# Optimization experiments

Measured on AMD Instinct MI355X. Metric: run time of the kernel, lower is better.

## Reference

```python
import jax, jax.numpy as jnp
import numpy as np

EPS = 1e-5  # config.layer_norm_epsilon

def setup_inputs() -> dict:
    key = jax.random.key(0)
    ks = jax.random.split(key, 8)
    B, S, D, BOT, N = 8, 2048, 1024, 400, 25
    x = jax.random.normal(ks[0], (B, S, D), dtype=jnp.float32)
    alphas = jax.random.uniform(ks[1], (N,), dtype=jnp.float32) / N
    W_down_all = jax.random.normal(ks[2], (N, BOT, D), dtype=jnp.float32) * 0.02
    W_up_all = jax.random.normal(ks[3], (N, D, BOT), dtype=jnp.float32) * 0.02
    b_down_all = jax.random.normal(ks[4], (N, BOT), dtype=jnp.float32) * 0.02
    b_up_all = jax.random.normal(ks[5], (N, D), dtype=jnp.float32) * 0.02
    W_ln_all = 1.0 + jax.random.normal(ks[6], (N, D), dtype=jnp.float32) * 0.02
    b_ln_all = jax.random.normal(ks[7], (N, D), dtype=jnp.float32) * 0.02
    return {"x": x, "alphas": alphas, "W_down_all": W_down_all, "W_up_all": W_up_all,
            "b_down_all": b_down_all, "b_up_all": b_up_all,
            "W_ln_all": W_ln_all, "b_ln_all": b_ln_all}

def reference(x, alphas, W_down_all, W_up_all, b_down_all, b_up_all, W_ln_all, b_ln_all):
    # Superposition: alpha-weighted sum of all adapters' parameters
    # (original python loop over 25 adapters -> single einsum per tensor).
    W_down = jnp.einsum('n,nbd->bd', alphas, W_down_all)  # [BOT, D]
    W_up   = jnp.einsum('n,ndb->db', alphas, W_up_all)    # [D, BOT]
    W_ln   = jnp.einsum('n,nd->d',  alphas, W_ln_all)     # [D]
    b_ln   = jnp.einsum('n,nd->d',  alphas, b_ln_all)     # [D]
    # b_up / b_down are merged in the original too but passed with bias=None: unused.

    # FAdapter: F.layer_norm with normalized_shape = x.shape[1:], i.e. normalize
    # jointly over (seq, embd) per batch element; ln weight/bias broadcast over seq.
    mu = jnp.mean(x, axis=(1, 2), keepdims=True)
    var = jnp.mean(jnp.square(x - mu), axis=(1, 2), keepdims=True)
    x_ = (x - mu) * jax.lax.rsqrt(var + EPS) * W_ln + b_ln  # [B,S,D]

    h = jax.nn.relu(jnp.einsum('bsd,od->bso', x_, W_down))  # [B,S,BOT], no bias
    x_ = jnp.einsum('bso,do->bsd', h, W_up)                 # [B,S,D],   no bias
    return x + x_
```

## Files before the change

### kernel.cpp

```cpp
#include <hip/hip_runtime.h>
#include <stdint.h>

#define NB   8
#define SS   2048
#define DD   1024
#define BOT  400
#define BOTP 512
#define NAD  25
#define LN_EPS 1e-5f
#define NCH  128

typedef __attribute__((ext_vector_type(8))) short bf8_t;
typedef __attribute__((ext_vector_type(4))) float fx4;

__device__ __forceinline__ unsigned short f2bf(float f) {
  unsigned int u = __float_as_uint(f);
  u = (u + 0x7FFFu + ((u >> 16) & 1u)) >> 16;
  return (unsigned short)u;
}
__device__ __forceinline__ uint32_t cvtpk(float lo, float hi) {
  uint32_t r;
  asm("v_cvt_pk_bf16_f32 %0, %1, %2" : "=v"(r) : "v"(lo), "v"(hi));
  return r;
}

__device__ __forceinline__ void gload16(void* lds, const void* g) {
  __builtin_amdgcn_global_load_lds(
      (const __attribute__((address_space(1))) void*)(uintptr_t)g,
      (__attribute__((address_space(3))) void*)(uint32_t)(uintptr_t)lds,
      16, 0, 0);
}

__global__ __launch_bounds__(256) void mix_kernel(
    const float* __restrict__ alphas,
    const float* __restrict__ WdAll, const float* __restrict__ WuAll,
    const float* __restrict__ wlnAll, const float* __restrict__ blnAll,
    unsigned short* __restrict__ Wd, unsigned short* __restrict__ Wu,
    float* __restrict__ wln, float* __restrict__ bln)
{
  __shared__ float a[NAD];
  const int tid = threadIdx.x;
  if (tid < NAD) a[tid] = alphas[tid];
  __syncthreads();
  const int bid = blockIdx.x;

  if (bid < 800) {
    const int g = (bid < 400 ? bid : bid - 400) * 256 + tid;
    const float4* src = (const float4*)(bid < 400 ? WdAll : WuAll) + g;
    float4 vals[NAD];
#pragma unroll
    for (int n = 0; n < NAD; ++n) vals[n] = src[(size_t)n * 102400];
    float4 acc = {0.f, 0.f, 0.f, 0.f};
#pragma unroll
    for (int n = 0; n < NAD; ++n) {
      acc.x += a[n] * vals[n].x; acc.y += a[n] * vals[n].y;
      acc.z += a[n] * vals[n].z; acc.w += a[n] * vals[n].w;
    }
    uint2 pk = { cvtpk(acc.x, acc.y), cvtpk(acc.z, acc.w) };
    if (bid < 400) {
      *(uint2*)(Wd + (size_t)g * 4) = pk;
    } else {
      const int d = g / 100, bg = g - d * 100;
      *(uint2*)(Wu + (size_t)d * BOTP + bg * 4) = pk;
    }
  } else if (bid < 808) {
    const int i = (bid - 800) * 256 + tid;
    const float* src = (i < DD) ? wlnAll : blnAll;
    const int j = (i < DD) ? i : (i - DD);
    float v[NAD];
#pragma unroll
    for (int n = 0; n < NAD; ++n) v[n] = src[(size_t)n * DD + j];
    float s = 0.f;
#pragma unroll
    for (int n = 0; n < NAD; ++n) s += a[n] * v[n];
    if (i < DD) wln[j] = s; else bln[j] = s;
  } else if (bid < 864) {
    const int t = (bid - 808) * 256 + tid;
    int4 z = {0, 0, 0, 0};
    *(int4*)(Wd + 400 * 1024 + (size_t)t * 8) = z;
  } else {
    const int t = (bid - 864) * 256 + tid;
    const int row = t / 14, c8 = t - row * 14;
    int4 z = {0, 0, 0, 0};
    *(int4*)(Wu + (size_t)row * BOTP + 400 + c8 * 8) = z;
  }
}

__global__ __launch_bounds__(256) void stats_kernel(const float* __restrict__ x,
                                                    float* __restrict__ partials)
{
  const int b = blockIdx.y, c = blockIdx.x;
  const float4* xb = (const float4*)(x + (size_t)b * SS * DD) + (size_t)c * 4096;
  float s = 0.f, q = 0.f;
#pragma unroll 4
  for (int i = threadIdx.x; i < 4096; i += 256) {
    float4 v = xb[i];
    s += v.x + v.y + v.z + v.w;
    q += v.x * v.x + v.y * v.y + v.z * v.z + v.w * v.w;
  }
#pragma unroll
  for (int off = 32; off > 0; off >>= 1) { s += __shfl_down(s, off); q += __shfl_down(q, off); }
  __shared__ float red[8];
  const int wave = threadIdx.x >> 6, lane = threadIdx.x & 63;
  if (!lane) { red[wave] = s; red[wave + 4] = q; }
  __syncthreads();
  if (!threadIdx.x) {
    partials[(b * NCH + c) * 2]     = red[0] + red[1] + red[2] + red[3];
    partials[(b * NCH + c) * 2 + 1] = red[4] + red[5] + red[6] + red[7];
  }
}

__global__ __launch_bounds__(256) void gemm1(
    const float* __restrict__ x, const unsigned short* __restrict__ Bw,
    const float* __restrict__ partials, const float* __restrict__ wln,
    const float* __restrict__ bln, unsigned short* __restrict__ H)
{
  __shared__ unsigned short As[2][128 * 64];
  __shared__ unsigned short Bs[2][128 * 64];
  __shared__ float s1[DD], s2[DD];
  const int tid = threadIdx.x, wave = tid >> 6, lane = tid & 63;
  const int wr = wave >> 1, wc = wave & 1;
  const int bid = (blockIdx.x & 7) * 64 + (blockIdx.x >> 3);
  const int bcol = bid & 3, brow = bid >> 2;
  const int b = brow >> 4;

  double sd = 0.0, qd = 0.0;
#pragma unroll 8
  for (int i = 0; i < NCH; ++i) {
    sd += partials[(b * NCH + i) * 2];
    qd += partials[(b * NCH + i) * 2 + 1];
  }
  const float mu  = (float)(sd * (1.0 / 2097152.0));
  const float var = (float)(qd * (1.0 / 2097152.0)) - mu * mu;
  const float rs  = rsqrtf(var + LN_EPS);
  for (int c = tid; c < DD; c += 256) {
    const float v1 = rs * wln[c];
    s1[c] = v1; s2[c] = bln[c] - mu * v1;
  }

  const float* Ab = x + (size_t)(brow * 128) * DD;
  const unsigned short* Bb = Bw + (size_t)(bcol * 128) * DD;
  const int arow = tid >> 3;
  const int c8   = tid & 7;
  const int aswz = (arow & 7) << 4;

  auto loadA = [&](int k0, float4* xr) {
#pragma unroll
    for (int i = 0; i < 4; ++i) {
      const float* p = Ab + (size_t)(i * 32 + arow) * DD + k0 + c8 * 8;
      xr[i * 2]     = *(const float4*)p;
      xr[i * 2 + 1] = *(const float4*)(p + 4);
    }
  };
  auto writeA = [&](int buf, int k0, const float4* xr) {
    const float4 w0 = *(const float4*)&s1[k0 + c8 * 8];
    const float4 w1 = *(const float4*)&s1[k0 + c8 * 8 + 4];
    const float4 b0 = *(const float4*)&s2[k0 + c8 * 8];
    const float4 b1 = *(const float4*)&s2[k0 + c8 * 8 + 4];
#pragma unroll
    for (int i = 0; i < 4; ++i) {
      const float4 v0 = xr[i * 2], v1 = xr[i * 2 + 1];
      uint4 pk;
      pk.x = cvtpk(v0.x * w0.x + b0.x, v0.y * w0.y + b0.y);
      pk.y = cvtpk(v0.z * w0.z + b0.z, v0.w * w0.w + b0.w);
      pk.z = cvtpk(v1.x * w1.x + b1.x, v1.y * w1.y + b1.y);
      pk.w = cvtpk(v1.z * w1.z + b1.z, v1.w * w1.w + b1.w);
      *(uint4*)((char*)&As[buf][0] + (i * 32 + arow) * 128 + ((c8 * 16) ^ aswz)) = pk;
    }
  };
  auto stageB = [&](int buf, int k0) {
#pragma unroll
    for (int i = 0; i < 4; ++i) {
      const int q   = i * 256 + wave * 64;
      const int ql  = q + lane;
      const int row = ql >> 3, c16 = ql & 7;
      const int o   = c16 ^ (row & 7);
      gload16(&Bs[buf][q * 8], Bb + (size_t)row * DD + k0 + o * 8);
    }
  };

  fx4 acc[4][4] = {};
  auto compute = [&](int buf) {
#pragma unroll
    for (int kk = 0; kk < 2; ++kk) {
      bf8_t af[4], bf[4];
#pragma unroll
      for (int m = 0; m < 4; ++m) {
        const int r = wr * 64 + m * 16 + (lane & 15);
        af[m] = *(const bf8_t*)((const char*)&As[buf][0] + r * 128 +
                                ((kk * 64 + (lane >> 4) * 16) ^ ((r & 7) << 4)));
      }
#pragma unroll
      for (int n = 0; n < 4; ++n) {
        const int r = wc * 64 + n * 16 + (lane & 15);
        bf[n] = *(const bf8_t*)((const char*)&Bs[buf][0] + r * 128 +
                                ((kk * 64 + (lane >> 4) * 16) ^ ((r & 7) << 4)));
      }
#pragma unroll
      for (int m = 0; m < 4; ++m)
#pragma unroll
        for (int n = 0; n < 4; ++n)
          acc[m][n] = __builtin_amdgcn_mfma_f32_16x16x32_bf16(af[m], bf[n], acc[m][n], 0, 0, 0);
    }
  };

  float4 xrA[8], xrB[8];
  loadA(0, xrA); stageB(0, 0);
  __syncthreads();
  writeA(0, 0, xrA);
  __syncthreads();
#pragma unroll 1
  for (int t2 = 0; t2 < 8; ++t2) {
    {
      const int t = t2 * 2;
      if (t < 15) { loadA((t + 1) * 64, xrB); stageB(1, (t + 1) * 64); }
      compute(0);
      if (t < 15) writeA(1, (t + 1) * 64, xrB);
      __syncthreads();
    }
    {
      const int t = t2 * 2 + 1;
      if (t < 15) { loadA((t + 1) * 64, xrA); stageB(0, (t + 1) * 64); }
      compute(1);
      if (t < 15) writeA(0, (t + 1) * 64, xrA);
      __syncthreads();
    }
  }

  unsigned short* Hs = &As[0][0];
  const int r0l = wr * 64 + ((lane >> 4) << 2);
  const int c0l = wc * 64 + (lane & 15);
#pragma unroll
  for (int m = 0; m < 4; ++m)
#pragma unroll
    for (int n = 0; n < 4; ++n)
#pragma unroll
      for (int j = 0; j < 4; ++j) {
        float v = acc[m][n][j];
        Hs[(r0l + m * 16 + j) * 128 + (c0l + n * 16)] = f2bf(v > 0.f ? v : 0.f);
      }
  __syncthreads();
  const size_t outbase = (size_t)(brow * 128) * BOTP + (size_t)bcol * 128;
#pragma unroll
  for (int i = 0; i < 8; ++i) {
    const int idx = i * 256 + tid;
    const int row = idx >> 4, colg = idx & 15;
    *(int4*)(H + outbase + (size_t)row * BOTP + colg * 8) = *(const int4*)&Hs[row * 128 + colg * 8];
  }
}

__global__ __launch_bounds__(256) void gemm2(
    const unsigned short* __restrict__ A, const unsigned short* __restrict__ Bm,
    const float* __restrict__ Xres, float* __restrict__ out)
{
  __shared__ unsigned short As[2][128 * 32];
  __shared__ unsigned short Bs[2][128 * 32];
  const int tid = threadIdx.x, wave = tid >> 6, lane = tid & 63;
  const int wr = wave >> 1, wc = wave & 1;
  const int bid = (blockIdx.x & 7) * 128 + (blockIdx.x >> 3);
  const int bcol = bid & 7, brow = bid >> 3;
  const unsigned short* Ab = A + (size_t)(brow * 128) * BOTP;
  const unsigned short* Bb = Bm + (size_t)(bcol * 128) * BOTP;

  auto stage = [&](int buf, int k0) {
#pragma unroll
    for (int i = 0; i < 2; ++i) {
      const int q   = i * 256 + wave * 64;
      const int ql  = q + lane;
      const int row = ql >> 2, c16 = ql & 3;
      const int o   = c16 ^ (row & 3);
      gload16(&As[buf][q * 8], Ab + (size_t)row * BOTP + k0 + o * 8);
      gload16(&Bs[buf][q * 8], Bb + (size_t)row * BOTP + k0 + o * 8);
    }
  };

  fx4 acc[4][4] = {};
  stage(0, 0);
  __syncthreads();
  for (int t = 0; t < 16; ++t) {
    const int cur = t & 1;
    if (t < 15) stage(cur ^ 1, (t + 1) * 32);
    bf8_t af[4], bf[4];
    const int hi16 = (lane >> 4) * 16;
#pragma unroll
    for (int m = 0; m < 4; ++m) {
      const int r = wr * 64 + m * 16 + (lane & 15);
      af[m] = *(const bf8_t*)((const char*)&As[cur][0] + r * 64 + (hi16 ^ ((r & 3) << 4)));
    }
#pragma unroll
    for (int n = 0; n < 4; ++n) {
      const int r = wc * 64 + n * 16 + (lane & 15);
      bf[n] = *(const bf8_t*)((const char*)&Bs[cur][0] + r * 64 + (hi16 ^ ((r & 3) << 4)));
    }
#pragma unroll
    for (int m = 0; m < 4; ++m)
#pragma unroll
      for (int n = 0; n < 4; ++n)
        acc[m][n] = __builtin_amdgcn_mfma_f32_16x16x32_bf16(af[m], bf[n], acc[m][n], 0, 0, 0);
    __syncthreads();
  }

  const int r0 = brow * 128 + wr * 64 + ((lane >> 4) << 2);
  const int c0 = bcol * 128 + wc * 64 + (lane & 15);
#pragma unroll
  for (int m = 0; m < 4; ++m)
#pragma unroll
    for (int n = 0; n < 4; ++n)
#pragma unroll
      for (int j = 0; j < 4; ++j) {
        const size_t off = (size_t)(r0 + m * 16 + j) * DD + (c0 + n * 16);
        out[off] = acc[m][n][j] + Xres[off];
      }
}

extern "C" void kernel_launch(void* const* d_in, const int* in_sizes, int n_in,
                              void* d_out, int out_size, void* d_ws, size_t ws_size,
                              hipStream_t stream)
{
  const float* x      = (const float*)d_in[0];
  const float* alphas = (const float*)d_in[1];
  const float* WdAll  = (const float*)d_in[2];
  const float* WuAll  = (const float*)d_in[3];
  const float* wlnAll = (const float*)d_in[6];
  const float* blnAll = (const float*)d_in[7];
  float* out = (float*)d_out;

  char* ws = (char*)d_ws;
  unsigned short* Wd  = (unsigned short*)ws;
  unsigned short* Wu  = (unsigned short*)(ws + (1u << 20));
  float* wln          = (float*)(ws + (2u << 20));
  float* bln          = wln + DD;
  float* partials     = bln + DD;
  unsigned short* h   = (unsigned short*)(ws + (3u << 20));

  mix_kernel<<<920, 256, 0, stream>>>(alphas, WdAll, WuAll, wlnAll, blnAll, Wd, Wu, wln, bln);
  stats_kernel<<<dim3(NCH, NB), 256, 0, stream>>>(x, partials);
  gemm1<<<512, 256, 0, stream>>>(x, Wd, partials, wln, bln, h);
  gemm2<<<1024, 256, 0, stream>>>(h, Wu, x, out);
}
```

Before: 274.7 us.

## Fuse mix and stats kernels, shrink GEMM K-tiles, drop swizzle and remapping

Merges the weight-mixing and LayerNorm statistics kernels into one launch so the x reduction and the adapter mixing share a grid. gemm1 moves from a 64-wide double-buffered K tile to a 32-wide single-buffered LDS tile with register prefetch of A. gemm2 becomes single-buffered with a sync per K step. Both GEMMs lose their XOR LDS swizzle and their XCD-aware block remapping. These changes cut launches and LDS footprint but risk bank conflicts, more barriers and worse L2 locality.

```diff
diff --git a/kernel.cpp b/kernel.cpp
--- a/kernel.cpp
+++ b/kernel.cpp
@@ -31,18 +31,45 @@
       16, 0, 0);
 }
 
-__global__ __launch_bounds__(256) void mix_kernel(
+__global__ __launch_bounds__(256) void mixstats_kernel(
     const float* __restrict__ alphas,
     const float* __restrict__ WdAll, const float* __restrict__ WuAll,
     const float* __restrict__ wlnAll, const float* __restrict__ blnAll,
+    const float* __restrict__ x,
     unsigned short* __restrict__ Wd, unsigned short* __restrict__ Wu,
-    float* __restrict__ wln, float* __restrict__ bln)
+    float* __restrict__ wln, float* __restrict__ bln,
+    float* __restrict__ partials)
 {
+  const int tid = threadIdx.x;
+  const int bid = blockIdx.x;
+
+  if (bid >= 920) {
+    const int g = bid - 920;
+    const int b = g >> 7, c = g & 127;
+    const float4* xb = (const float4*)(x + (size_t)b * SS * DD) + (size_t)c * 4096;
+    float s = 0.f, q = 0.f;
+#pragma unroll 4
+    for (int i = tid; i < 4096; i += 256) {
+      float4 v = xb[i];
+      s += v.x + v.y + v.z + v.w;
+      q += v.x * v.x + v.y * v.y + v.z * v.z + v.w * v.w;
+    }
+#pragma unroll
+    for (int off = 32; off > 0; off >>= 1) { s += __shfl_down(s, off); q += __shfl_down(q, off); }
+    __shared__ float red[8];
+    const int wave = tid >> 6, lane = tid & 63;
+    if (!lane) { red[wave] = s; red[wave + 4] = q; }
+    __syncthreads();
+    if (!tid) {
+      partials[(b * NCH + c) * 2]     = red[0] + red[1] + red[2] + red[3];
+      partials[(b * NCH + c) * 2 + 1] = red[4] + red[5] + red[6] + red[7];
+    }
+    return;
+  }
+
   __shared__ float a[NAD];
-  const int tid = threadIdx.x;
   if (tid < NAD) a[tid] = alphas[tid];
   __syncthreads();
-  const int bid = blockIdx.x;
 
   if (bid < 800) {
     const int g = (bid < 400 ? bid : bid - 400) * 256 + tid;
@@ -86,42 +113,20 @@
   }
 }
 
-__global__ __launch_bounds__(256) void stats_kernel(const float* __restrict__ x,
-                                                    float* __restrict__ partials)
-{
-  const int b = blockIdx.y, c = blockIdx.x;
-  const float4* xb = (const float4*)(x + (size_t)b * SS * DD) + (size_t)c * 4096;
-  float s = 0.f, q = 0.f;
-#pragma unroll 4
-  for (int i = threadIdx.x; i < 4096; i += 256) {
-    float4 v = xb[i];
-    s += v.x + v.y + v.z + v.w;
-    q += v.x * v.x + v.y * v.y + v.z * v.z + v.w * v.w;
-  }
-#pragma unroll
-  for (int off = 32; off > 0; off >>= 1) { s += __shfl_down(s, off); q += __shfl_down(q, off); }
-  __shared__ float red[8];
-  const int wave = threadIdx.x >> 6, lane = threadIdx.x & 63;
-  if (!lane) { red[wave] = s; red[wave + 4] = q; }
-  __syncthreads();
-  if (!threadIdx.x) {
-    partials[(b * NCH + c) * 2]     = red[0] + red[1] + red[2] + red[3];
-    partials[(b * NCH + c) * 2 + 1] = red[4] + red[5] + red[6] + red[7];
-  }
-}
-
 __global__ __launch_bounds__(256) void gemm1(
-    const float* __restrict__ x, const unsigned short* __restrict__ Bw,
+    const float* __restrict__ x, const unsigned short* __restrict__ Wdm,
     const float* __restrict__ partials, const float* __restrict__ wln,
     const float* __restrict__ bln, unsigned short* __restrict__ H)
 {
-  __shared__ unsigned short As[2][128 * 64];
-  __shared__ unsigned short Bs[2][128 * 64];
-  __shared__ float s1[DD], s2[DD];
+  __shared__ char smraw[32768];
+  unsigned short* As = (unsigned short*)smraw;
+  unsigned short* Bs = (unsigned short*)(smraw + 8192);
+  float* s1 = (float*)(smraw + 16384);
+  float* s2 = (float*)(smraw + 20480);
+
   const int tid = threadIdx.x, wave = tid >> 6, lane = tid & 63;
   const int wr = wave >> 1, wc = wave & 1;
-  const int bid = (blockIdx.x & 7) * 64 + (blockIdx.x >> 3);
-  const int bcol = bid & 3, brow = bid >> 2;
+  const int bcol = blockIdx.x & 3, brow = blockIdx.x >> 2;
   const int b = brow >> 4;
 
   double sd = 0.0, qd = 0.0;
@@ -139,95 +144,91 @@
   }
 
   const float* Ab = x + (size_t)(brow * 128) * DD;
-  const unsigned short* Bb = Bw + (size_t)(bcol * 128) * DD;
-  const int arow = tid >> 3;
-  const int c8   = tid & 7;
-  const int aswz = (arow & 7) << 4;
+  const unsigned short* Bb = Wdm + (size_t)(bcol * 128) * DD;
+  const int row2 = tid >> 1;
+  const int c16  = (tid & 1) * 16;
 
   auto loadA = [&](int k0, float4* xr) {
-#pragma unroll
-    for (int i = 0; i < 4; ++i) {
-      const float* p = Ab + (size_t)(i * 32 + arow) * DD + k0 + c8 * 8;
-      xr[i * 2]     = *(const float4*)p;
-      xr[i * 2 + 1] = *(const float4*)(p + 4);
-    }
+    const float* p = Ab + (size_t)row2 * DD + k0 + c16;
+    xr[0] = *(const float4*)p;     xr[1] = *(const float4*)(p + 4);
+    xr[2] = *(const float4*)(p + 8); xr[3] = *(const float4*)(p + 12);
   };
-  auto writeA = [&](int buf, int k0, const float4* xr) {
-    const float4 w0 = *(const float4*)&s1[k0 + c8 * 8];
-    const float4 w1 = *(const float4*)&s1[k0 + c8 * 8 + 4];
-    const float4 b0 = *(const float4*)&s2[k0 + c8 * 8];
-    const float4 b1 = *(const float4*)&s2[k0 + c8 * 8 + 4];
-#pragma unroll
-    for (int i = 0; i < 4; ++i) {
-      const float4 v0 = xr[i * 2], v1 = xr[i * 2 + 1];
-      uint4 pk;
-      pk.x = cvtpk(v0.x * w0.x + b0.x, v0.y * w0.y + b0.y);
-      pk.y = cvtpk(v0.z * w0.z + b0.z, v0.w * w0.w + b0.w);
-      pk.z = cvtpk(v1.x * w1.x + b1.x, v1.y * w1.y + b1.y);
-      pk.w = cvtpk(v1.z * w1.z + b1.z, v1.w * w1.w + b1.w);
-      *(uint4*)((char*)&As[buf][0] + (i * 32 + arow) * 128 + ((c8 * 16) ^ aswz)) = pk;
-    }
+  auto writeA = [&](int k0, const float4* xr) {
+    const float4 wA = *(const float4*)&s1[k0 + c16],      wB = *(const float4*)&s1[k0 + c16 + 4];
+    const float4 wC = *(const float4*)&s1[k0 + c16 + 8],  wD = *(const float4*)&s1[k0 + c16 + 12];
+    const float4 bA = *(const float4*)&s2[k0 + c16],      bB = *(const float4*)&s2[k0 + c16 + 4];
+    const float4 bC = *(const float4*)&s2[k0 + c16 + 8],  bD = *(const float4*)&s2[k0 + c16 + 12];
+    uint4 p0, p1;
+    p0.x = cvtpk(xr[0].x * wA.x + bA.x, xr[0].y * wA.y + bA.y);
+    p0.y = cvtpk(xr[0].z * wA.z + bA.z, xr[0].w * wA.w + bA.w);
+    p0.z = cvtpk(xr[1].x * wB.x + bB.x, xr[1].y * wB.y + bB.y);
+    p0.w = cvtpk(xr[1].z * wB.z + bB.z, xr[1].w * wB.w + bB.w);
+    p1.x = cvtpk(xr[2].x * wC.x + bC.x, xr[2].y * wC.y + bC.y);
+    p1.y = cvtpk(xr[2].z * wC.z + bC.z, xr[2].w * wC.w + bC.w);
+    p1.z = cvtpk(xr[3].x * wD.x + bD.x, xr[3].y * wD.y + bD.y);
+    p1.w = cvtpk(xr[3].z * wD.z + bD.z, xr[3].w * wD.w + bD.w);
+    *(uint4*)&As[row2 * 32 + c16]     = p0;
+    *(uint4*)&As[row2 * 32 + c16 + 8] = p1;
   };
-  auto stageB = [&](int buf, int k0) {
-#pragma unroll
-    for (int i = 0; i < 4; ++i) {
-      const int q   = i * 256 + wave * 64;
-      const int ql  = q + lane;
-      const int row = ql >> 3, c16 = ql & 7;
-      const int o   = c16 ^ (row & 7);
-      gload16(&Bs[buf][q * 8], Bb + (size_t)row * DD + k0 + o * 8);
+  auto stageB = [&](int k0) {
+#pragma unroll
+    for (int i = 0; i < 2; ++i) {
+      const int basee = (i * 256 + wave * 64) * 8;
+      const int e   = basee + lane * 8;
+      const int row = e >> 5, col = e & 31;
+      gload16(&Bs[basee], Bb + (size_t)row * DD + k0 + col);
     }
   };
 
   fx4 acc[4][4] = {};
-  auto compute = [&](int buf) {
-#pragma unroll
-    for (int kk = 0; kk < 2; ++kk) {
-      bf8_t af[4], bf[4];
-#pragma unroll
-      for (int m = 0; m < 4; ++m) {
-        const int r = wr * 64 + m * 16 + (lane & 15);
-        af[m] = *(const bf8_t*)((const char*)&As[buf][0] + r * 128 +
-                                ((kk * 64 + (lane >> 4) * 16) ^ ((r & 7) << 4)));
-      }
-#pragma unroll
-      for (int n = 0; n < 4; ++n) {
-        const int r = wc * 64 + n * 16 + (lane & 15);
-        bf[n] = *(const bf8_t*)((const char*)&Bs[buf][0] + r * 128 +
-                                ((kk * 64 + (lane >> 4) * 16) ^ ((r & 7) << 4)));
-      }
-#pragma unroll
-      for (int m = 0; m < 4; ++m)
-#pragma unroll
-        for (int n = 0; n < 4; ++n)
-          acc[m][n] = __builtin_amdgcn_mfma_f32_16x16x32_bf16(af[m], bf[n], acc[m][n], 0, 0, 0);
-    }
+  auto compute = [&]() {
+    bf8_t af[4], bf[4];
+    const int hi8 = (lane >> 4) * 8;
+#pragma unroll
+    for (int m = 0; m < 4; ++m)
+      af[m] = *(const bf8_t*)&As[(wr * 64 + m * 16 + (lane & 15)) * 32 + hi8];
+#pragma unroll
+    for (int n = 0; n < 4; ++n)
+      bf[n] = *(const bf8_t*)&Bs[(wc * 64 + n * 16 + (lane & 15)) * 32 + hi8];
+#pragma unroll
+    for (int m = 0; m < 4; ++m)
+#pragma unroll
+      for (int n = 0; n < 4; ++n)
+        acc[m][n] = __builtin_amdgcn_mfma_f32_16x16x32_bf16(af[m], bf[n], acc[m][n], 0, 0, 0);
   };
 
-  float4 xrA[8], xrB[8];
-  loadA(0, xrA); stageB(0, 0);
+  float4 xrA[4], xrB[4];
+  loadA(0, xrA); stageB(0); loadA(32, xrB);
   __syncthreads();
-  writeA(0, 0, xrA);
+  writeA(0, xrA);
   __syncthreads();
 #pragma unroll 1
-  for (int t2 = 0; t2 < 8; ++t2) {
+  for (int t2 = 0; t2 < 16; ++t2) {
     {
       const int t = t2 * 2;
-      if (t < 15) { loadA((t + 1) * 64, xrB); stageB(1, (t + 1) * 64); }
-      compute(0);
-      if (t < 15) writeA(1, (t + 1) * 64, xrB);
+      compute();
+      __syncthreads();
+      if (t < 31) {
+        stageB((t + 1) * 32);
+        writeA((t + 1) * 32, xrB);
+        if (t + 2 < 32) loadA((t + 2) * 32, xrA);
+      }
       __syncthreads();
     }
     {
       const int t = t2 * 2 + 1;
-      if (t < 15) { loadA((t + 1) * 64, xrA); stageB(0, (t + 1) * 64); }
-      compute(1);
-      if (t < 15) writeA(0, (t + 1) * 64, xrA);
+      compute();
       __syncthreads();
-    }
-  }
-
-  unsigned short* Hs = &As[0][0];
+      if (t < 31) {
+        stageB((t + 1) * 32);
+        writeA((t + 1) * 32, xrA);
+        if (t + 2 < 32) loadA((t + 2) * 32, xrB);
+      }
+      __syncthreads();
+    }
+  }
+
+  unsigned short* Hs = (unsigned short*)smraw;
   const int r0l = wr * 64 + ((lane >> 4) << 2);
   const int c0l = wc * 64 + (lane & 15);
 #pragma unroll
@@ -253,45 +254,33 @@
     const unsigned short* __restrict__ A, const unsigned short* __restrict__ Bm,
     const float* __restrict__ Xres, float* __restrict__ out)
 {
-  __shared__ unsigned short As[2][128 * 32];
-  __shared__ unsigned short Bs[2][128 * 32];
+  __shared__ unsigned short As[128 * 32];
+  __shared__ unsigned short Bs[128 * 32];
   const int tid = threadIdx.x, wave = tid >> 6, lane = tid & 63;
   const int wr = wave >> 1, wc = wave & 1;
-  const int bid = (blockIdx.x & 7) * 128 + (blockIdx.x >> 3);
-  const int bcol = bid & 7, brow = bid >> 3;
+  const int bcol = blockIdx.x & 7, brow = blockIdx.x >> 3;
   const unsigned short* Ab = A + (size_t)(brow * 128) * BOTP;
   const unsigned short* Bb = Bm + (size_t)(bcol * 128) * BOTP;
 
-  auto stage = [&](int buf, int k0) {
+  fx4 acc[4][4] = {};
+  for (int k0 = 0; k0 < 512; k0 += 32) {
 #pragma unroll
     for (int i = 0; i < 2; ++i) {
-      const int q   = i * 256 + wave * 64;
-      const int ql  = q + lane;
-      const int row = ql >> 2, c16 = ql & 3;
-      const int o   = c16 ^ (row & 3);
-      gload16(&As[buf][q * 8], Ab + (size_t)row * BOTP + k0 + o * 8);
-      gload16(&Bs[buf][q * 8], Bb + (size_t)row * BOTP + k0 + o * 8);
-    }
-  };
-
-  fx4 acc[4][4] = {};
-  stage(0, 0);
-  __syncthreads();
-  for (int t = 0; t < 16; ++t) {
-    const int cur = t & 1;
-    if (t < 15) stage(cur ^ 1, (t + 1) * 32);
+      const int basee = (i * 256 + wave * 64) * 8;
+      const int e   = basee + lane * 8;
+      const int row = e >> 5, col = e & 31;
+      gload16(&As[basee], Ab + (size_t)row * BOTP + k0 + col);
+      gload16(&Bs[basee], Bb + (size_t)row * BOTP + k0 + col);
+    }
+    __syncthreads();
     bf8_t af[4], bf[4];
-    const int hi16 = (lane >> 4) * 16;
-#pragma unroll
-    for (int m = 0; m < 4; ++m) {
-      const int r = wr * 64 + m * 16 + (lane & 15);
-      af[m] = *(const bf8_t*)((const char*)&As[cur][0] + r * 64 + (hi16 ^ ((r & 3) << 4)));
-    }
-#pragma unroll
-    for (int n = 0; n < 4; ++n) {
-      const int r = wc * 64 + n * 16 + (lane & 15);
-      bf[n] = *(const bf8_t*)((const char*)&Bs[cur][0] + r * 64 + (hi16 ^ ((r & 3) << 4)));
-    }
+    const int hi8 = (lane >> 4) * 8;
+#pragma unroll
+    for (int m = 0; m < 4; ++m)
+      af[m] = *(const bf8_t*)&As[(wr * 64 + m * 16 + (lane & 15)) * 32 + hi8];
+#pragma unroll
+    for (int n = 0; n < 4; ++n)
+      bf[n] = *(const bf8_t*)&Bs[(wc * 64 + n * 16 + (lane & 15)) * 32 + hi8];
 #pragma unroll
     for (int m = 0; m < 4; ++m)
 #pragma unroll
@@ -333,8 +322,8 @@
   float* partials     = bln + DD;
   unsigned short* h   = (unsigned short*)(ws + (3u << 20));
 
-  mix_kernel<<<920, 256, 0, stream>>>(alphas, WdAll, WuAll, wlnAll, blnAll, Wd, Wu, wln, bln);
-  stats_kernel<<<dim3(NCH, NB), 256, 0, stream>>>(x, partials);
+  mixstats_kernel<<<1944, 256, 0, stream>>>(alphas, WdAll, WuAll, wlnAll, blnAll, x,
+                                            Wd, Wu, wln, bln, partials);
   gemm1<<<512, 256, 0, stream>>>(x, Wd, partials, wln, bln, h);
   gemm2<<<1024, 256, 0, stream>>>(h, Wu, x, out);
 }
```

New measurement: 275.2 us. Within noise of the previous version (+0.2%).
